# Optimization experiments

Measured on AMD Instinct MI355X. Metric: run time of the kernel, lower is better.

The kernel has to match this reference:

```python
import jax, jax.numpy as jnp
import numpy as np

B, S, D = 4, 4096, 1024
BLOCK_LEN = 128
NUM_BLOCKS = S // BLOCK_LEN  # 32


def setup_inputs() -> dict:
    key = jax.random.key(0)
    k0, k1, k2 = jax.random.split(key, 3)
    x = jax.random.normal(k0, (B, S, D), dtype=jnp.float32)
    # nn.Linear weights stored as (in, out) for x @ W + b convention
    Wqkv = jax.random.normal(k1, (D, 3 * D), dtype=jnp.float32) * (1.0 / np.sqrt(D))
    bqkv = jnp.zeros((3 * D,), dtype=jnp.float32)
    Wout = jax.random.normal(k2, (D, D), dtype=jnp.float32) * (1.0 / np.sqrt(D))
    bout = jnp.zeros((D,), dtype=jnp.float32)
    return {"x": x, "Wqkv": Wqkv, "bqkv": bqkv, "Wout": Wout, "bout": bout}


def _causal_attn(q, k, v):
    # q,k,v: (..., L, D); single-head SDPA with scale 1/sqrt(D), causal mask
    d = q.shape[-1]
    L = q.shape[-2]
    scale = 1.0 / np.sqrt(d)
    scores = jnp.einsum('...qd,...kd->...qk', q, k) * jnp.asarray(scale, q.dtype)
    mask = jnp.tril(jnp.ones((L, L), dtype=bool))
    neg = jnp.asarray(jnp.finfo(scores.dtype).min, scores.dtype)
    scores = jnp.where(mask, scores, neg)
    p = jax.nn.softmax(scores, axis=-1)
    return jnp.einsum('...qk,...kd->...qd', p, v)


def reference(x, Wqkv, bqkv, Wout, bout):
    b, s, d = x.shape
    nb = s // BLOCK_LEN
    x2 = x.reshape(b, nb, BLOCK_LEN, d)              # (B, NB, BL, D)
    qkv = x2 @ Wqkv + bqkv                            # (B, NB, BL, 3D)
    q, k, v = jnp.split(qkv, 3, axis=-1)
    # 'column' attention: attend across blocks at the same within-block position
    q = q.transpose(0, 2, 1, 3)                       # (B, BL, NB, D)
    k = k.transpose(0, 2, 1, 3)
    v = v.transpose(0, 2, 1, 3)
    out = _causal_attn(q, k, v)                       # (B, BL, NB, D)
    out = out.transpose(0, 2, 1, 3).reshape(b, s, d)  # back to (B, S, D)
    return out @ Wout + bout
```

## Files before the change

kernel.cpp:

```cpp
#include <hip/hip_runtime.h>
#include <math.h>

#define BB   4
#define SS   4096
#define DD   1024
#define BL   128
#define NB   32

typedef __attribute__((ext_vector_type(4))) float f32x4;
typedef __attribute__((ext_vector_type(16))) float f32x16;
typedef __attribute__((ext_vector_type(8))) short bf16x8;
typedef __attribute__((ext_vector_type(8))) unsigned short u16x8;

__device__ __forceinline__ float bf2f(unsigned short u) {
    return __uint_as_float(((unsigned int)u) << 16);
}
__device__ __forceinline__ unsigned short f2bf(float f) {
    unsigned int u = __float_as_uint(f);
    return (unsigned short)((u + 0x7FFFu + ((u >> 16) & 1u)) >> 16);
}
__device__ __forceinline__ void gload_lds16(const unsigned short* g, unsigned short* l) {
    __builtin_amdgcn_global_load_lds(
        (const __attribute__((address_space(1))) void*)g,
        (__attribute__((address_space(3))) void*)l, 16, 0, 0);
}

__global__ __launch_bounds__(256) void cvt_f32_bf16(const float4* __restrict__ in,
                                                    ushort4* __restrict__ out, int n4) {
    int i = blockIdx.x * 256 + threadIdx.x;
    if (i < n4) {
        float4 v = in[i];
        ushort4 o;
        o.x = f2bf(v.x); o.y = f2bf(v.y); o.z = f2bf(v.z); o.w = f2bf(v.w);
        out[i] = o;
    }
}

__global__ __launch_bounds__(256) void transcvt(const float* __restrict__ W,
                                                unsigned short* __restrict__ WT,
                                                int K, int N) {
    __shared__ float tile[32][33];
    const int n0 = blockIdx.x * 32, k0 = blockIdx.y * 32;
    const int tx = threadIdx.x & 31, ty = threadIdx.x >> 5;
    #pragma unroll
    for (int r = 0; r < 32; r += 8)
        tile[ty + r][tx] = W[(size_t)(k0 + ty + r) * N + n0 + tx];
    __syncthreads();
    #pragma unroll
    for (int r = 0; r < 32; r += 8)
        WT[(size_t)(n0 + ty + r) * K + k0 + tx] = f2bf(tile[tx][ty + r]);
}


#define GBAR() __builtin_amdgcn_s_barrier()
#define LGKM(n) do { asm volatile("s_waitcnt lgkmcnt(" #n ")" ::: "memory"); \
                     __builtin_amdgcn_sched_barrier(0); } while (0)

#define MFMA_PAIR2(AR, q, ni) \
    acc[(q)*2+0][ni] = __builtin_amdgcn_mfma_f32_16x16x32_bf16(AR[0][0], bC[ni][0], acc[(q)*2+0][ni], 0, 0, 0); \
    acc[(q)*2+0][ni] = __builtin_amdgcn_mfma_f32_16x16x32_bf16(AR[0][1], bC[ni][1], acc[(q)*2+0][ni], 0, 0, 0); \
    acc[(q)*2+1][ni] = __builtin_amdgcn_mfma_f32_16x16x32_bf16(AR[1][0], bC[ni][0], acc[(q)*2+1][ni], 0, 0, 0); \
    acc[(q)*2+1][ni] = __builtin_amdgcn_mfma_f32_16x16x32_bf16(AR[1][1], bC[ni][1], acc[(q)*2+1][ni], 0, 0, 0);

#define MFMA_Q(AR, q) do { \
    __builtin_amdgcn_s_setprio(1); \
    MFMA_PAIR2(AR, q, 0) MFMA_PAIR2(AR, q, 1) \
    MFMA_PAIR2(AR, q, 2) MFMA_PAIR2(AR, q, 3) \
    __builtin_amdgcn_s_setprio(0); } while (0)

#define READ_AQ(dst, pA_, q) do { \
    dst[0][0] = *(const bf16x8*)((pA_) + ((q)*2+0)*1024 + sw0); \
    dst[0][1] = *(const bf16x8*)((pA_) + ((q)*2+0)*1024 + sw1); \
    dst[1][0] = *(const bf16x8*)((pA_) + ((q)*2+1)*1024 + sw0); \
    dst[1][1] = *(const bf16x8*)((pA_) + ((q)*2+1)*1024 + sw1); } while (0)

#define READ_B8(pB_) do { \
    bC[0][0] = *(const bf16x8*)((pB_) + 0*1024 + sw0); \
    bC[0][1] = *(const bf16x8*)((pB_) + 0*1024 + sw1); \
    bC[1][0] = *(const bf16x8*)((pB_) + 1*1024 + sw0); \
    bC[1][1] = *(const bf16x8*)((pB_) + 1*1024 + sw1); \
    bC[2][0] = *(const bf16x8*)((pB_) + 2*1024 + sw0); \
    bC[2][1] = *(const bf16x8*)((pB_) + 2*1024 + sw1); \
    bC[3][0] = *(const bf16x8*)((pB_) + 3*1024 + sw0); \
    bC[3][1] = *(const bf16x8*)((pB_) + 3*1024 + sw1); } while (0)

template<typename OutT>
__global__ __launch_bounds__(512, 1) void gemm256(
    const unsigned short* __restrict__ A, const unsigned short* __restrict__ BT,
    const float* __restrict__ bias, OutT* __restrict__ C,
    int M, int N, int K, int ntn)
{
    __shared__ __align__(16) unsigned short smem[65536];
    unsigned short* sAb = smem;
    unsigned short* sBb = smem + 32768;

    const int nwg = gridDim.x;
    const int wg  = blockIdx.x;
    const int swzb = (wg & 7) * (nwg >> 3) + (wg >> 3);
    const int m0 = (swzb / ntn) * 256, n0 = (swzb % ntn) * 256;

    const int t    = threadIdx.x;
    const int w    = t >> 6;
    const int lane = t & 63;
    const int wm   = w >> 2, wn = w & 3;

    const int srow8 = lane >> 3;
    const int sgch  = (lane & 7) ^ srow8;
    const int NT    = K >> 6;

    auto STAGE_A = [&](int ts, int cb) {
        const int r = cb + (w << 3);
        gload_lds16(A + (size_t)(m0 + r + srow8) * K + (ts << 6) + sgch * 8,
                    sAb + (size_t)(ts & 1) * 16384 + r * 64);
    };
    auto STAGE_B = [&](int ts, int cb) {
        const int r = cb + (w << 3);
        gload_lds16(BT + (size_t)(n0 + r + srow8) * K + (ts << 6) + sgch * 8,
                    sBb + (size_t)(ts & 1) * 16384 + r * 64);
    };

    const int frA = wm * 128 + (lane & 15);
    const int frB = wn * 64  + (lane & 15);
    const int sw0 = (((lane >> 4) + 0) ^ (lane & 7)) * 8;
    const int sw1 = (((lane >> 4) + 4) ^ (lane & 7)) * 8;

    f32x4 acc[8][4];
    #pragma unroll
    for (int i = 0; i < 8; ++i)
        #pragma unroll
        for (int j = 0; j < 4; ++j) acc[i][j] = (f32x4){0.f, 0.f, 0.f, 0.f};

    bf16x8 bC[4][2];
    bf16x8 aX[2][2], aY[2][2];

    STAGE_B(0, 0); STAGE_B(0, 64); STAGE_B(0, 128); STAGE_B(0, 192);
    STAGE_A(0, 0); STAGE_A(0, 64); STAGE_A(0, 128); STAGE_A(0, 192);
    if (NT > 1) {
        STAGE_B(1, 0); STAGE_B(1, 64); STAGE_B(1, 128); STAGE_B(1, 192);
        STAGE_A(1, 0); STAGE_A(1, 128);
        asm volatile("s_waitcnt vmcnt(6)" ::: "memory");
    } else {
        asm volatile("s_waitcnt vmcnt(0)" ::: "memory");
    }
    GBAR();
    READ_AQ(aX, sAb + frA * 64, 0);

    for (int ts = 0; ts < NT; ++ts) {
        const unsigned short* pAc = sAb + (size_t)(ts & 1) * 16384 + frA * 64;
        const unsigned short* pAn = sAb + (size_t)((ts + 1) & 1) * 16384 + frA * 64;
        const unsigned short* pBc = sBb + (size_t)(ts & 1) * 16384 + frB * 64;

        READ_B8(pBc);
        READ_AQ(aY, pAc, 1);
        if (ts + 1 < NT) { STAGE_A(ts + 1, 64); STAGE_A(ts + 1, 192); }
        LGKM(4); MFMA_Q(aX, 0); GBAR();

        READ_AQ(aX, pAc, 2);
        if (ts + 2 < NT) { STAGE_B(ts + 2, 0); STAGE_B(ts + 2, 64); }
        LGKM(4); MFMA_Q(aY, 1); GBAR();

        READ_AQ(aY, pAc, 3);
        if (ts + 2 < NT) { STAGE_B(ts + 2, 128); STAGE_B(ts + 2, 192); }
        LGKM(4); MFMA_Q(aX, 2); GBAR();

        if (ts + 1 < NT) {
            if (ts + 2 < NT) { asm volatile("s_waitcnt vmcnt(4)" ::: "memory"); }
            else             { asm volatile("s_waitcnt vmcnt(0)" ::: "memory"); }
            READ_AQ(aX, pAn, 0);
            if (ts + 2 < NT) { STAGE_A(ts + 2, 0); STAGE_A(ts + 2, 128); }
            LGKM(4); MFMA_Q(aY, 3);
        } else {
            LGKM(0); MFMA_Q(aY, 3);
        }
        GBAR();
    }

    if constexpr (sizeof(OutT) == 2) {
        unsigned short (*cb)[256] = (unsigned short (*)[256])smem;
        #pragma unroll
        for (int ni = 0; ni < 4; ++ni) {
            const int col = wn * 64 + ni * 16 + (lane & 15);
            const float bv = bias[n0 + col];
            #pragma unroll
            for (int mi = 0; mi < 8; ++mi) {
                const int rb = wm * 128 + mi * 16 + ((lane >> 4) << 2);
                #pragma unroll
                for (int r = 0; r < 4; ++r)
                    cb[rb + r][col] = f2bf(acc[mi][ni][r] + bv);
            }
        }
        __syncthreads();
        unsigned short* Cp = (unsigned short*)C;
        #pragma unroll
        for (int it = 0; it < 16; ++it) {
            const int row = it * 16 + (t >> 5);
            const int cs  = (t & 31) * 8;
            u16x8 v = *(const u16x8*)&cb[row][cs];
            *(u16x8*)(Cp + (size_t)(m0 + row) * N + n0 + cs) = v;
        }
    } else {
        float (*cf)[256] = (float (*)[256])smem;
        #pragma unroll
        for (int h = 0; h < 2; ++h) {
            if (wm == h) {
                #pragma unroll
                for (int ni = 0; ni < 4; ++ni) {
                    const int col = wn * 64 + ni * 16 + (lane & 15);
                    const float bv = bias[n0 + col];
                    #pragma unroll
                    for (int mi = 0; mi < 8; ++mi) {
                        const int rb = mi * 16 + ((lane >> 4) << 2);
                        #pragma unroll
                        for (int r = 0; r < 4; ++r)
                            cf[rb + r][col] = acc[mi][ni][r] + bv;
                    }
                }
            }
            __syncthreads();
            float* Cp = (float*)C;
            #pragma unroll
            for (int it = 0; it < 16; ++it) {
                const int row = it * 8 + (t >> 6);
                const int c4  = (t & 63) * 4;
                float4 v = *(const float4*)&cf[row][c4];
                *(float4*)(Cp + (size_t)(m0 + h * 128 + row) * N + n0 + c4) = v;
            }
            __syncthreads();
        }
    }
}

__global__ __launch_bounds__(512) void col_attn_mfma(const unsigned short* __restrict__ qkv,
                                                     unsigned short* __restrict__ outb)
{
    const int b  = blockIdx.x >> 7;
    const int bl = blockIdx.x & (BL - 1);

    __shared__ float red[8][32][33];
    __shared__ float p_s[NB][NB + 1];

    const int t    = threadIdx.x;
    const int w    = t >> 6;
    const int lane = t & 63;

    const size_t rowstride = (size_t)BL * 3 * DD;
    const unsigned short* base = qkv + ((size_t)b * NB * BL + bl) * (3 * DD);

    {
        const int arow = lane & 31;
        const int khi  = (lane >> 5) * 8;
        const unsigned short* qp = base + (size_t)arow * rowstride + w * 128 + khi;
        const unsigned short* kp = qp + DD;

        f32x16 acc0 = {}, acc1 = {};
        #pragma unroll
        for (int s = 0; s < 8; s += 2) {
            bf16x8 aq0 = *(const bf16x8*)(qp + s * 16);
            bf16x8 bk0 = *(const bf16x8*)(kp + s * 16);
            bf16x8 aq1 = *(const bf16x8*)(qp + s * 16 + 16);
            bf16x8 bk1 = *(const bf16x8*)(kp + s * 16 + 16);
            acc0 = __builtin_amdgcn_mfma_f32_32x32x16_bf16(aq0, bk0, acc0, 0, 0, 0);
            acc1 = __builtin_amdgcn_mfma_f32_32x32x16_bf16(aq1, bk1, acc1, 0, 0, 0);
        }
        const int ccol = lane & 31;
        const int rhi  = (lane >> 5) * 4;
        #pragma unroll
        for (int r = 0; r < 16; ++r) {
            const int crow = (r & 3) + 8 * (r >> 2) + rhi;
            red[w][crow][ccol] = acc0[r] + acc1[r];
        }
    }
    __syncthreads();

    {
        const float scale = 1.0f / 32.0f;
        const int row = t >> 4;
        const int c0  = (t & 15) * 2;
        #pragma unroll
        for (int j = 0; j < 2; ++j) {
            const int c = c0 + j;
            float s = red[0][row][c];
            #pragma unroll
            for (int ww = 1; ww < 8; ++ww) s += red[ww][row][c];
            p_s[row][c] = s * scale;
        }
    }
    __syncthreads();

    if (t < NB) {
        const int i = t;
        float mx = p_s[i][0];
        for (int j = 1; j <= i; ++j) mx = fmaxf(mx, p_s[i][j]);
        float sum = 0.f;
        for (int j = 0; j <= i; ++j) { float e = __expf(p_s[i][j] - mx); p_s[i][j] = e; sum += e; }
        const float inv = 1.0f / sum;
        for (int j = 0; j <= i; ++j) p_s[i][j] *= inv;
        for (int j = i + 1; j < NB; ++j) p_s[i][j] = 0.f;
    }
    __syncthreads();

    const int grp = t >> 8;
    const int tt  = t & 255;
    const int d0v = tt * 4;
    const unsigned short* vbase = base + 2 * DD;
    const int passes[2][2] = {{0, 3}, {1, 2}};
    #pragma unroll
    for (int pi = 0; pi < 2; ++pi) {
        const int p = passes[grp][pi];
        float4 accv[8];
        #pragma unroll
        for (int ii = 0; ii < 8; ++ii) accv[ii] = make_float4(0.f, 0.f, 0.f, 0.f);
        const int jmax = (p + 1) * 8;
        for (int j = 0; j < jmax; ++j) {
            ushort4 v4 = *(const ushort4*)(vbase + (size_t)j * rowstride + d0v);
            const float vx = bf2f(v4.x), vy = bf2f(v4.y), vz = bf2f(v4.z), vw = bf2f(v4.w);
            #pragma unroll
            for (int ii = 0; ii < 8; ++ii) {
                const float pij = p_s[p * 8 + ii][j];
                accv[ii].x += pij * vx;
                accv[ii].y += pij * vy;
                accv[ii].z += pij * vz;
                accv[ii].w += pij * vw;
            }
        }
        #pragma unroll
        for (int ii = 0; ii < 8; ++ii) {
            const int i = p * 8 + ii;
            ushort4 o;
            o.x = f2bf(accv[ii].x); o.y = f2bf(accv[ii].y);
            o.z = f2bf(accv[ii].z); o.w = f2bf(accv[ii].w);
            *(ushort4*)(outb + ((size_t)(b * NB + i) * BL + bl) * DD + d0v) = o;
        }
    }
}

extern "C" void kernel_launch(void* const* d_in, const int* in_sizes, int n_in,
                              void* d_out, int out_size, void* d_ws, size_t ws_size,
                              hipStream_t stream) {
    (void)in_sizes; (void)n_in; (void)out_size; (void)ws_size;
    const float* x    = (const float*)d_in[0];
    const float* Wqkv = (const float*)d_in[1];
    const float* bqkv = (const float*)d_in[2];
    const float* Wout = (const float*)d_in[3];
    const float* bout = (const float*)d_in[4];
    float* out = (float*)d_out;

    char* ws = (char*)d_ws;
    unsigned short* xb    = (unsigned short*)ws;
    unsigned short* WqkvT = (unsigned short*)(ws + ((size_t)32 << 20));
    unsigned short* WoutT = (unsigned short*)(ws + ((size_t)38 << 20));
    unsigned short* qkvb  = (unsigned short*)(ws + ((size_t)40 << 20));
    unsigned short* attnb = (unsigned short*)(ws + ((size_t)136 << 20));

    const int M = BB * SS;

    cvt_f32_bf16<<<dim3((M * DD / 4 + 255) / 256), dim3(256), 0, stream>>>(
        (const float4*)x, (ushort4*)xb, M * DD / 4);
    transcvt<<<dim3(3 * DD / 32, DD / 32), dim3(256), 0, stream>>>(Wqkv, WqkvT, DD, 3 * DD);
    transcvt<<<dim3(DD / 32, DD / 32), dim3(256), 0, stream>>>(Wout, WoutT, DD, DD);

    gemm256<unsigned short><<<dim3((M / 256) * (3 * DD / 256)), dim3(512), 0, stream>>>(
        xb, WqkvT, bqkv, qkvb, M, 3 * DD, DD, 3 * DD / 256);

    col_attn_mfma<<<dim3(BB * BL), dim3(512), 0, stream>>>(qkvb, attnb);

    gemm256<float><<<dim3((M / 256) * (DD / 256)), dim3(512), 0, stream>>>(
        attnb, WoutT, bout, out, M, DD, DD, DD / 256);
}
```

Baseline: 208.7 us.

## Replace double-buffered A register pipeline with single buffer and extra barriers

Drops the aX/aY ping-pong A-fragment registers, so the LDS reads of each quarter no longer overlap the MFMAs of the previous quarter. Each quarter now waits for lgkmcnt(0) and adds an extra workgroup barrier. The vmcnt wait points are moved as well. This lowers VGPR pressure and simplifies ordering, but it serialises LDS reads with MFMA work and doubles the number of barriers per k-step.

```diff
diff --git a/kernel.cpp b/kernel.cpp
--- a/kernel.cpp
+++ b/kernel.cpp
@@ -53,26 +53,25 @@
 
 
 #define GBAR() __builtin_amdgcn_s_barrier()
-#define LGKM(n) do { asm volatile("s_waitcnt lgkmcnt(" #n ")" ::: "memory"); \
-                     __builtin_amdgcn_sched_barrier(0); } while (0)
-
-#define MFMA_PAIR2(AR, q, ni) \
-    acc[(q)*2+0][ni] = __builtin_amdgcn_mfma_f32_16x16x32_bf16(AR[0][0], bC[ni][0], acc[(q)*2+0][ni], 0, 0, 0); \
-    acc[(q)*2+0][ni] = __builtin_amdgcn_mfma_f32_16x16x32_bf16(AR[0][1], bC[ni][1], acc[(q)*2+0][ni], 0, 0, 0); \
-    acc[(q)*2+1][ni] = __builtin_amdgcn_mfma_f32_16x16x32_bf16(AR[1][0], bC[ni][0], acc[(q)*2+1][ni], 0, 0, 0); \
-    acc[(q)*2+1][ni] = __builtin_amdgcn_mfma_f32_16x16x32_bf16(AR[1][1], bC[ni][1], acc[(q)*2+1][ni], 0, 0, 0);
-
-#define MFMA_Q(AR, q) do { \
+#define WAIT_LGKM0() asm volatile("s_waitcnt lgkmcnt(0)" ::: "memory")
+#define WAIT_LGKM8() asm volatile("s_waitcnt lgkmcnt(8)" ::: "memory")
+
+#define MFMA_PAIR2(q, ni) \
+    acc[(q)*2+0][ni] = __builtin_amdgcn_mfma_f32_16x16x32_bf16(aC[0][0], bC[ni][0], acc[(q)*2+0][ni], 0, 0, 0); \
+    acc[(q)*2+0][ni] = __builtin_amdgcn_mfma_f32_16x16x32_bf16(aC[0][1], bC[ni][1], acc[(q)*2+0][ni], 0, 0, 0); \
+    acc[(q)*2+1][ni] = __builtin_amdgcn_mfma_f32_16x16x32_bf16(aC[1][0], bC[ni][0], acc[(q)*2+1][ni], 0, 0, 0); \
+    acc[(q)*2+1][ni] = __builtin_amdgcn_mfma_f32_16x16x32_bf16(aC[1][1], bC[ni][1], acc[(q)*2+1][ni], 0, 0, 0);
+
+#define MFMA_Q(q) do { \
     __builtin_amdgcn_s_setprio(1); \
-    MFMA_PAIR2(AR, q, 0) MFMA_PAIR2(AR, q, 1) \
-    MFMA_PAIR2(AR, q, 2) MFMA_PAIR2(AR, q, 3) \
+    MFMA_PAIR2(q, 0) MFMA_PAIR2(q, 1) MFMA_PAIR2(q, 2) MFMA_PAIR2(q, 3) \
     __builtin_amdgcn_s_setprio(0); } while (0)
 
-#define READ_AQ(dst, pA_, q) do { \
-    dst[0][0] = *(const bf16x8*)((pA_) + ((q)*2+0)*1024 + sw0); \
-    dst[0][1] = *(const bf16x8*)((pA_) + ((q)*2+0)*1024 + sw1); \
-    dst[1][0] = *(const bf16x8*)((pA_) + ((q)*2+1)*1024 + sw0); \
-    dst[1][1] = *(const bf16x8*)((pA_) + ((q)*2+1)*1024 + sw1); } while (0)
+#define READ_AQ(pA_, q) do { \
+    aC[0][0] = *(const bf16x8*)((pA_) + ((q)*2+0)*1024 + sw0); \
+    aC[0][1] = *(const bf16x8*)((pA_) + ((q)*2+0)*1024 + sw1); \
+    aC[1][0] = *(const bf16x8*)((pA_) + ((q)*2+1)*1024 + sw0); \
+    aC[1][1] = *(const bf16x8*)((pA_) + ((q)*2+1)*1024 + sw1); } while (0)
 
 #define READ_B8(pB_) do { \
     bC[0][0] = *(const bf16x8*)((pB_) + 0*1024 + sw0); \
@@ -131,10 +130,11 @@
         for (int j = 0; j < 4; ++j) acc[i][j] = (f32x4){0.f, 0.f, 0.f, 0.f};
 
     bf16x8 bC[4][2];
-    bf16x8 aX[2][2], aY[2][2];
+    bf16x8 aC[2][2];
 
     STAGE_B(0, 0); STAGE_B(0, 64); STAGE_B(0, 128); STAGE_B(0, 192);
     STAGE_A(0, 0); STAGE_A(0, 64); STAGE_A(0, 128); STAGE_A(0, 192);
+    asm volatile("s_waitcnt vmcnt(4)" ::: "memory");
     if (NT > 1) {
         STAGE_B(1, 0); STAGE_B(1, 64); STAGE_B(1, 128); STAGE_B(1, 192);
         STAGE_A(1, 0); STAGE_A(1, 128);
@@ -143,35 +143,30 @@
         asm volatile("s_waitcnt vmcnt(0)" ::: "memory");
     }
     GBAR();
-    READ_AQ(aX, sAb + frA * 64, 0);
 
     for (int ts = 0; ts < NT; ++ts) {
         const unsigned short* pAc = sAb + (size_t)(ts & 1) * 16384 + frA * 64;
-        const unsigned short* pAn = sAb + (size_t)((ts + 1) & 1) * 16384 + frA * 64;
         const unsigned short* pBc = sBb + (size_t)(ts & 1) * 16384 + frB * 64;
 
         READ_B8(pBc);
-        READ_AQ(aY, pAc, 1);
+        READ_AQ(pAc, 0);
         if (ts + 1 < NT) { STAGE_A(ts + 1, 64); STAGE_A(ts + 1, 192); }
-        LGKM(4); MFMA_Q(aX, 0); GBAR();
-
-        READ_AQ(aX, pAc, 2);
+        WAIT_LGKM8();
+        GBAR(); WAIT_LGKM0(); MFMA_Q(0); GBAR();
+
+        READ_AQ(pAc, 1);
         if (ts + 2 < NT) { STAGE_B(ts + 2, 0); STAGE_B(ts + 2, 64); }
-        LGKM(4); MFMA_Q(aY, 1); GBAR();
-
-        READ_AQ(aY, pAc, 3);
+        GBAR(); WAIT_LGKM0(); MFMA_Q(1); GBAR();
+
+        READ_AQ(pAc, 2);
         if (ts + 2 < NT) { STAGE_B(ts + 2, 128); STAGE_B(ts + 2, 192); }
-        LGKM(4); MFMA_Q(aX, 2); GBAR();
-
-        if (ts + 1 < NT) {
-            if (ts + 2 < NT) { asm volatile("s_waitcnt vmcnt(4)" ::: "memory"); }
-            else             { asm volatile("s_waitcnt vmcnt(0)" ::: "memory"); }
-            READ_AQ(aX, pAn, 0);
-            if (ts + 2 < NT) { STAGE_A(ts + 2, 0); STAGE_A(ts + 2, 128); }
-            LGKM(4); MFMA_Q(aY, 3);
-        } else {
-            LGKM(0); MFMA_Q(aY, 3);
-        }
+        GBAR(); WAIT_LGKM0(); MFMA_Q(2); GBAR();
+
+        READ_AQ(pAc, 3);
+        if (ts + 2 < NT) { STAGE_A(ts + 2, 0); STAGE_A(ts + 2, 128); }
+        GBAR(); WAIT_LGKM0(); MFMA_Q(3);
+        if (ts + 2 < NT) { asm volatile("s_waitcnt vmcnt(6)" ::: "memory"); }
+        else             { asm volatile("s_waitcnt vmcnt(0)" ::: "memory"); }
         GBAR();
     }
 
```

Result: slower. 213.7 us (+2.4%).
